# Optimization experiments

Measured on AMD Instinct MI355X. Metric: run time of the kernel, lower is better.

## Reference

```python
import jax, jax.numpy as jnp
import numpy as np

B, S, D_IN, D_OUT = 4, 2048, 1024, 1024


def setup_inputs() -> dict:
    key = jax.random.key(0)
    kx, kq, kk, kv = jax.random.split(key, 4)
    scale = 1.0 / np.sqrt(D_IN)
    return {
        "x": jax.random.normal(kx, (B, S, D_IN), dtype=jnp.float32),
        "W_q": jax.random.normal(kq, (D_IN, D_OUT), dtype=jnp.float32) * scale,
        "W_k": jax.random.normal(kk, (D_IN, D_OUT), dtype=jnp.float32) * scale,
        "W_v": jax.random.normal(kv, (D_IN, D_OUT), dtype=jnp.float32) * scale,
    }


def reference(x, W_q, W_k, W_v):
    # QKV projections (Linear without bias): [B,S,D_out]
    q = jnp.einsum("bsd,de->bse", x, W_q)
    k = jnp.einsum("bsd,de->bse", x, W_k)
    v = jnp.einsum("bsd,de->bse", x, W_v)

    # Raw scores [B,S,S], causal mask (strict upper triangle -> -inf),
    # then scale by sqrt(d_k) and softmax, matching the torch order of ops.
    scores = jnp.einsum("bqd,bkd->bqk", q, k)
    seq = scores.shape[-1]
    causal = jnp.triu(jnp.ones((seq, seq), dtype=bool), k=1)
    scores = jnp.where(causal[None, :, :], -jnp.inf, scores)
    attn = jax.nn.softmax(scores / jnp.sqrt(jnp.asarray(q.shape[-1], scores.dtype)), axis=-1)
    # dropout p=0.0 -> identity (eval semantics)
    return jnp.einsum("bqk,bkd->bqd", attn, v)
```

## Files before the change

### kernel.cpp

```cpp
#include <hip/hip_runtime.h>

typedef unsigned short u16;
typedef __bf16 bf16x8 __attribute__((ext_vector_type(8)));
typedef float f32x4 __attribute__((ext_vector_type(4)));

__device__ __forceinline__ u16 f2bf(float f) {
    union { float f; unsigned int u; } v; v.f = f;
    unsigned int u = v.u;
    return (u16)((u + 0x7FFFu + ((u >> 16) & 1u)) >> 16);
}

__device__ __forceinline__ void load_lds16(const void* g, void* l) {
    __builtin_amdgcn_global_load_lds(
        (const __attribute__((address_space(1))) unsigned int*)g,
        (__attribute__((address_space(3))) unsigned int*)l,
        16, 0, 0);
}

__global__ void __launch_bounds__(256) prep_kernel(
    const float4* __restrict__ X, u16* __restrict__ xb,
    const float* __restrict__ Wq, const float* __restrict__ Wk,
    const float* __restrict__ Wv,
    u16* __restrict__ Oq, u16* __restrict__ Ok, u16* __restrict__ Ov,
    float* __restrict__ rowsum) {
    __shared__ float tile[32][33];
    const int bid = blockIdx.x, tid = threadIdx.x;
    if (bid < 8192) {
        int idx = bid * 256 + tid;
        float4 v = X[idx];
        ushort4 o;
        o.x = f2bf(v.x); o.y = f2bf(v.y); o.z = f2bf(v.z); o.w = f2bf(v.w);
        *(ushort4*)(xb + (size_t)idx * 4) = o;
    } else if (bid < 11264) {
        int id = bid - 8192;
        int zz = id >> 10;
        const float* W = (zz == 0) ? Wq : (zz == 1) ? Wk : Wv;
        u16* O = (zz == 0) ? Oq : (zz == 1) ? Ok : Ov;
        int n0 = (id & 31) * 32, k0 = ((id >> 5) & 31) * 32;
        int tx = tid & 31, ty = tid >> 5;
        #pragma unroll
        for (int j = 0; j < 32; j += 8)
            tile[ty + j][tx] = W[(size_t)(k0 + ty + j) * 1024 + n0 + tx];
        __syncthreads();
        #pragma unroll
        for (int j = 0; j < 32; j += 8)
            O[(size_t)(n0 + ty + j) * 1024 + k0 + tx] = f2bf(tile[tx][ty + j]);
    } else {
        rowsum[(bid - 11264) * 256 + tid] = 0.f;
    }
}

__global__ void __launch_bounds__(512) gemm_qkv(
    const u16* __restrict__ xb, const u16* __restrict__ WqT,
    const u16* __restrict__ WkT, const u16* __restrict__ WvT,
    u16* __restrict__ Q, u16* __restrict__ Kb, u16* __restrict__ Vt) {

    int L = blockIdx.x;
    int c = L & 7, t = (L >> 3) & 7, hi = L >> 6;
    int p = hi * 8 + c;
    const int z = p >> 6, mtile = p & 63, ntile = t;
    const u16* A = xb;
    const u16* B = (z == 0) ? WqT : (z == 1) ? WkT : WvT;

    __shared__ __align__(16) u16 As[2 * 128 * 32];
    __shared__ __align__(16) u16 Bs[2 * 128 * 32];

    const int tid = threadIdx.x;
    const int lane = tid & 63;
    const int wave = tid >> 6;
    const int wr = wave >> 2, wc = wave & 3;

    const int r0 = tid >> 2;
    const int kb = (((tid & 3) ^ ((r0 >> 1) & 3))) * 16;

    const char* gA = (const char*)(A + (size_t)(mtile * 128 + r0) * 1024) + kb;
    const char* gB = (const char*)(B + (size_t)(ntile * 128 + r0) * 1024) + kb;
    char* lA = (char*)As + tid * 16;
    char* lB = (char*)Bs + tid * 16;

    f32x4 acc[4][2] = {};

    const int quad = lane >> 4;
    const int l16 = lane & 15;
    const int ch = quad ^ ((l16 >> 1) & 3);
    const int aoff = (wr * 64 + l16) * 32 + ch * 8;
    const int boff = (wc * 32 + l16) * 32 + ch * 8;

    for (int kt = 0; kt < 16; ++kt) {
        load_lds16(gA,      lA);
        load_lds16(gA + 64, lA + 8192);
        load_lds16(gB,      lB);
        load_lds16(gB + 64, lB + 8192);
        gA += 128; gB += 128;
        __syncthreads();
        #pragma unroll
        for (int h = 0; h < 2; ++h) {
            const u16* ap = As + h * 4096 + aoff;
            const u16* bp = Bs + h * 4096 + boff;
            bf16x8 af[4], bfv[2];
            #pragma unroll
            for (int r = 0; r < 4; ++r) af[r] = *(const bf16x8*)(ap + r * 512);
            #pragma unroll
            for (int cc = 0; cc < 2; ++cc) bfv[cc] = *(const bf16x8*)(bp + cc * 512);
            #pragma unroll
            for (int r = 0; r < 4; ++r)
                #pragma unroll
                for (int cc = 0; cc < 2; ++cc)
                    acc[r][cc] = __builtin_amdgcn_mfma_f32_16x16x32_bf16(
                        af[r], bfv[cc], acc[r][cc], 0, 0, 0);
        }
        __syncthreads();
    }

    const int grow0 = mtile * 128 + wr * 64 + quad * 4;
    const int gcol0 = ntile * 128 + wc * 32 + l16;

    if (z < 2) {
        u16* C = z ? Kb : Q;
        #pragma unroll
        for (int r = 0; r < 4; ++r)
            #pragma unroll
            for (int cc = 0; cc < 2; ++cc)
                #pragma unroll
                for (int i = 0; i < 4; ++i)
                    C[(size_t)(grow0 + r * 16 + i) * 1024 + gcol0 + cc * 16] =
                        f2bf(acc[r][cc][i]);
    } else {
        #pragma unroll
        for (int r = 0; r < 4; ++r) {
            int m0 = grow0 + r * 16;
            int b = m0 >> 11, s0 = m0 & 2047;
            #pragma unroll
            for (int cc = 0; cc < 2; ++cc) {
                int d = gcol0 + cc * 16;
                ushort4 o;
                o.x = f2bf(acc[r][cc][0]); o.y = f2bf(acc[r][cc][1]);
                o.z = f2bf(acc[r][cc][2]); o.w = f2bf(acc[r][cc][3]);
                *(ushort4*)(Vt + (size_t)b * (1024 * 2048) + (size_t)d * 2048 + s0) = o;
            }
        }
    }
}

template <int MODE>
__global__ void __launch_bounds__(256) gemm_small(
    const u16* __restrict__ Q, const u16* __restrict__ Kb,
    const u16* __restrict__ Vt, u16* __restrict__ S,
    float* __restrict__ rowsum, float* __restrict__ out) {

    int g, ntile, z, kiters;
    const u16 *A, *B;

    if (MODE == 1) {
        int L = blockIdx.x;
        int p = L & 63;
        g = L >> 6;
        z = p >> 4;
        ntile = p & 15;
        if (ntile > (g >> 1)) return;
        kiters = 16;
        A = Q  + (size_t)z * (2048 * 1024);
        B = Kb + (size_t)z * (2048 * 1024);
    } else {
        int L = blockIdx.x;
        int p = L & 31;
        g = 31 - (L >> 5);
        z = p >> 3;
        ntile = p & 7;
        kiters = g + 1;
        A = S  + (size_t)z * (2048 * 2048);
        B = Vt + (size_t)z * (1024 * 2048);
    }

    const int LD = (MODE == 2) ? 2048 : 1024;

    __shared__ __align__(16) u16 As[2 * 64 * 32];
    __shared__ __align__(16) u16 Bs[2 * 128 * 32];

    const int tid = threadIdx.x;
    const int lane = tid & 63;
    const int wc = tid >> 6;
    const int r0 = tid >> 2;
    const int kb = (((tid & 3) ^ ((r0 >> 1) & 3))) * 16;

    const char* gA  = (const char*)(A + (size_t)(g * 64 + r0) * LD) + kb;
    const char* gB0 = (const char*)(B + (size_t)(ntile * 128 + r0) * LD) + kb;
    const char* gB1 = gB0 + (size_t)64 * LD * 2;

    char* lA = (char*)As + tid * 16;
    char* lB = (char*)Bs + tid * 16;

    f32x4 acc[4][2] = {};

    const int quad = lane >> 4;
    const int l16 = lane & 15;
    const int ch = quad ^ ((l16 >> 1) & 3);
    const int aoff = l16 * 32 + ch * 8;
    const int boff = (wc * 32 + l16) * 32 + ch * 8;

    for (int kt = 0; kt < kiters; ++kt) {
        #pragma unroll
        for (int h = 0; h < 2; ++h) {
            load_lds16(gA  + h * 64, lA + h * 4096);
            load_lds16(gB0 + h * 64, lB + h * 8192);
            load_lds16(gB1 + h * 64, lB + h * 8192 + 4096);
        }
        gA += 128; gB0 += 128; gB1 += 128;
        __syncthreads();
        #pragma unroll
        for (int h = 0; h < 2; ++h) {
            const u16* ap = As + h * 2048 + aoff;
            const u16* bp = Bs + h * 4096 + boff;
            bf16x8 af[4], bfv[2];
            #pragma unroll
            for (int r = 0; r < 4; ++r) af[r] = *(const bf16x8*)(ap + r * 512);
            #pragma unroll
            for (int cc = 0; cc < 2; ++cc) bfv[cc] = *(const bf16x8*)(bp + cc * 512);
            #pragma unroll
            for (int r = 0; r < 4; ++r)
                #pragma unroll
                for (int cc = 0; cc < 2; ++cc)
                    acc[r][cc] = __builtin_amdgcn_mfma_f32_16x16x32_bf16(
                        af[r], bfv[cc], acc[r][cc], 0, 0, 0);
        }
        __syncthreads();
    }

    const int grow0 = g * 64 + quad * 4;
    const int gcol0 = ntile * 128 + wc * 32 + l16;

    if (MODE == 1) {
        u16* C = S + (size_t)z * (2048 * 2048);
        float* rs = rowsum + z * 2048;
        float rsum[4][4];
        #pragma unroll
        for (int r = 0; r < 4; ++r)
            #pragma unroll
            for (int i = 0; i < 4; ++i) rsum[r][i] = 0.f;
        #pragma unroll
        for (int r = 0; r < 4; ++r)
            #pragma unroll
            for (int cc = 0; cc < 2; ++cc)
                #pragma unroll
                for (int i = 0; i < 4; ++i) {
                    int grow = grow0 + r * 16 + i;
                    int gcol = gcol0 + cc * 16;
                    float e = (gcol <= grow)
                                  ? __expf(acc[r][cc][i] * 0.03125f - 12.0f)
                                  : 0.f;
                    C[(size_t)grow * 2048 + gcol] = f2bf(e);
                    rsum[r][i] += e;
                }
        #pragma unroll
        for (int r = 0; r < 4; ++r)
            #pragma unroll
            for (int i = 0; i < 4; ++i) {
                float s = rsum[r][i];
                s += __shfl_xor(s, 1, 64);
                s += __shfl_xor(s, 2, 64);
                s += __shfl_xor(s, 4, 64);
                s += __shfl_xor(s, 8, 64);
                if (l16 == 0)
                    atomicAdd(&rs[grow0 + r * 16 + i], s);
            }
    } else {
        const float* rs = rowsum + z * 2048;
        float* C = out + (size_t)z * (2048 * 1024);
        #pragma unroll
        for (int r = 0; r < 4; ++r)
            #pragma unroll
            for (int i = 0; i < 4; ++i) {
                int grow = grow0 + r * 16 + i;
                float inv = 1.0f / rs[grow];
                #pragma unroll
                for (int cc = 0; cc < 2; ++cc)
                    C[(size_t)grow * 1024 + gcol0 + cc * 16] = acc[r][cc][i] * inv;
            }
    }
}

extern "C" void kernel_launch(void* const* d_in, const int* in_sizes, int n_in,
                              void* d_out, int out_size, void* d_ws, size_t ws_size,
                              hipStream_t stream) {
    const float* x  = (const float*)d_in[0];
    const float* Wq = (const float*)d_in[1];
    const float* Wk = (const float*)d_in[2];
    const float* Wv = (const float*)d_in[3];
    float* out = (float*)d_out;
    char* ws = (char*)d_ws;
    const size_t Mi = 1u << 20;

    u16* xb  = (u16*)(ws);
    u16* WqT = (u16*)(ws + 16 * Mi);
    u16* WkT = (u16*)(ws + 18 * Mi);
    u16* WvT = (u16*)(ws + 20 * Mi);
    u16* Q   = (u16*)(ws + 22 * Mi);
    u16* Kb  = (u16*)(ws + 38 * Mi);
    u16* Vt  = (u16*)(ws + 54 * Mi);
    u16* S   = (u16*)(ws + 70 * Mi);
    float* rowsum = (float*)(ws + 102 * Mi);

    prep_kernel<<<11296, 256, 0, stream>>>(
        (const float4*)x, xb, Wq, Wk, Wv, WqT, WkT, WvT, rowsum);

    gemm_qkv<<<1536, 512, 0, stream>>>(xb, WqT, WkT, WvT, Q, Kb, Vt);

    gemm_small<1><<<2048, 256, 0, stream>>>(Q, Kb, Vt, S, rowsum, out);

    gemm_small<2><<<1024, 256, 0, stream>>>(Q, Kb, Vt, S, rowsum, out);
}
```

Before: 246.5 us.

## Split scores and PV into dedicated kernels with 128x128 tiles and balanced causal scheduling

Replaces the templated 64x128-tile gemm_small with two 512-thread kernels using 128x128 tiles. The scores kernel enumerates only the lower-triangular tiles (544 blocks) through a paired mapping, and applies the causal mask only on diagonal tiles. The PV kernel gives each block two complementary row tiles (mtile and 15-mtile) so every block does the same amount of causal work. The goals are fewer wasted blocks, better operand reuse per load and balanced load, at the cost of fewer blocks in flight and more LDS per block.

After: 225.1 us. -8.7%, faster.

```diff
diff --git a/kernel.cpp b/kernel.cpp
--- a/kernel.cpp
+++ b/kernel.cpp
@@ -142,51 +142,34 @@
     }
 }
 
-template <int MODE>
-__global__ void __launch_bounds__(256) gemm_small(
+__global__ void __launch_bounds__(512) gemm_scores(
     const u16* __restrict__ Q, const u16* __restrict__ Kb,
-    const u16* __restrict__ Vt, u16* __restrict__ S,
-    float* __restrict__ rowsum, float* __restrict__ out) {
-
-    int g, ntile, z, kiters;
-    const u16 *A, *B;
-
-    if (MODE == 1) {
-        int L = blockIdx.x;
-        int p = L & 63;
-        g = L >> 6;
-        z = p >> 4;
-        ntile = p & 15;
-        if (ntile > (g >> 1)) return;
-        kiters = 16;
-        A = Q  + (size_t)z * (2048 * 1024);
-        B = Kb + (size_t)z * (2048 * 1024);
-    } else {
-        int L = blockIdx.x;
-        int p = L & 31;
-        g = 31 - (L >> 5);
-        z = p >> 3;
-        ntile = p & 7;
-        kiters = g + 1;
-        A = S  + (size_t)z * (2048 * 2048);
-        B = Vt + (size_t)z * (1024 * 2048);
-    }
-
-    const int LD = (MODE == 2) ? 2048 : 1024;
-
-    __shared__ __align__(16) u16 As[2 * 64 * 32];
+    u16* __restrict__ S, float* __restrict__ rowsum) {
+
+    const int L = blockIdx.x;
+    const int c = L & 7;
+    const int q = L >> 3;
+    const int z = q / 17;
+    const int j = q - z * 17;
+    const int mtile = (j <= c) ? c : 15 - c;
+    const int ntile = (j <= c) ? j : j - c - 1;
+
+    const u16* A = Q  + (size_t)z * (2048 * 1024);
+    const u16* B = Kb + (size_t)z * (2048 * 1024);
+
+    __shared__ __align__(16) u16 As[2 * 128 * 32];
     __shared__ __align__(16) u16 Bs[2 * 128 * 32];
 
     const int tid = threadIdx.x;
     const int lane = tid & 63;
-    const int wc = tid >> 6;
+    const int wave = tid >> 6;
+    const int wr = wave >> 2, wc = wave & 3;
+
     const int r0 = tid >> 2;
     const int kb = (((tid & 3) ^ ((r0 >> 1) & 3))) * 16;
 
-    const char* gA  = (const char*)(A + (size_t)(g * 64 + r0) * LD) + kb;
-    const char* gB0 = (const char*)(B + (size_t)(ntile * 128 + r0) * LD) + kb;
-    const char* gB1 = gB0 + (size_t)64 * LD * 2;
-
+    const char* gA = (const char*)(A + (size_t)(mtile * 128 + r0) * 1024) + kb;
+    const char* gB = (const char*)(B + (size_t)(ntile * 128 + r0) * 1024) + kb;
     char* lA = (char*)As + tid * 16;
     char* lB = (char*)Bs + tid * 16;
 
@@ -195,21 +178,19 @@
     const int quad = lane >> 4;
     const int l16 = lane & 15;
     const int ch = quad ^ ((l16 >> 1) & 3);
-    const int aoff = l16 * 32 + ch * 8;
+    const int aoff = (wr * 64 + l16) * 32 + ch * 8;
     const int boff = (wc * 32 + l16) * 32 + ch * 8;
 
-    for (int kt = 0; kt < kiters; ++kt) {
+    for (int kt = 0; kt < 16; ++kt) {
+        load_lds16(gA,      lA);
+        load_lds16(gA + 64, lA + 8192);
+        load_lds16(gB,      lB);
+        load_lds16(gB + 64, lB + 8192);
+        gA += 128; gB += 128;
+        __syncthreads();
         #pragma unroll
         for (int h = 0; h < 2; ++h) {
-            load_lds16(gA  + h * 64, lA + h * 4096);
-            load_lds16(gB0 + h * 64, lB + h * 8192);
-            load_lds16(gB1 + h * 64, lB + h * 8192 + 4096);
-        }
-        gA += 128; gB0 += 128; gB1 += 128;
-        __syncthreads();
-        #pragma unroll
-        for (int h = 0; h < 2; ++h) {
-            const u16* ap = As + h * 2048 + aoff;
+            const u16* ap = As + h * 4096 + aoff;
             const u16* bp = Bs + h * 4096 + boff;
             bf16x8 af[4], bfv[2];
             #pragma unroll
@@ -226,46 +207,118 @@
         __syncthreads();
     }
 
-    const int grow0 = g * 64 + quad * 4;
+    const int grow0 = mtile * 128 + wr * 64 + quad * 4;
     const int gcol0 = ntile * 128 + wc * 32 + l16;
 
-    if (MODE == 1) {
-        u16* C = S + (size_t)z * (2048 * 2048);
-        float* rs = rowsum + z * 2048;
-        float rsum[4][4];
-        #pragma unroll
-        for (int r = 0; r < 4; ++r)
-            #pragma unroll
-            for (int i = 0; i < 4; ++i) rsum[r][i] = 0.f;
-        #pragma unroll
-        for (int r = 0; r < 4; ++r)
-            #pragma unroll
-            for (int cc = 0; cc < 2; ++cc)
-                #pragma unroll
-                for (int i = 0; i < 4; ++i) {
-                    int grow = grow0 + r * 16 + i;
-                    int gcol = gcol0 + cc * 16;
-                    float e = (gcol <= grow)
-                                  ? __expf(acc[r][cc][i] * 0.03125f - 12.0f)
-                                  : 0.f;
-                    C[(size_t)grow * 2048 + gcol] = f2bf(e);
-                    rsum[r][i] += e;
-                }
-        #pragma unroll
-        for (int r = 0; r < 4; ++r)
+    u16* C = S + (size_t)z * (2048 * 2048);
+    float* rs = rowsum + z * 2048;
+    const bool diag = (ntile == mtile);
+    float rsum[4][4];
+    #pragma unroll
+    for (int r = 0; r < 4; ++r)
+        #pragma unroll
+        for (int i = 0; i < 4; ++i) rsum[r][i] = 0.f;
+    #pragma unroll
+    for (int r = 0; r < 4; ++r)
+        #pragma unroll
+        for (int cc = 0; cc < 2; ++cc)
             #pragma unroll
             for (int i = 0; i < 4; ++i) {
-                float s = rsum[r][i];
-                s += __shfl_xor(s, 1, 64);
-                s += __shfl_xor(s, 2, 64);
-                s += __shfl_xor(s, 4, 64);
-                s += __shfl_xor(s, 8, 64);
-                if (l16 == 0)
-                    atomicAdd(&rs[grow0 + r * 16 + i], s);
+                int grow = grow0 + r * 16 + i;
+                int gcol = gcol0 + cc * 16;
+                float e = 0.f;
+                if (!diag || gcol <= grow)
+                    e = __expf(acc[r][cc][i] * 0.03125f - 12.0f);
+                C[(size_t)grow * 2048 + gcol] = f2bf(e);
+                rsum[r][i] += e;
             }
-    } else {
-        const float* rs = rowsum + z * 2048;
-        float* C = out + (size_t)z * (2048 * 1024);
+    #pragma unroll
+    for (int r = 0; r < 4; ++r)
+        #pragma unroll
+        for (int i = 0; i < 4; ++i) {
+            float s = rsum[r][i];
+            s += __shfl_xor(s, 1, 64);
+            s += __shfl_xor(s, 2, 64);
+            s += __shfl_xor(s, 4, 64);
+            s += __shfl_xor(s, 8, 64);
+            if (l16 == 0)
+                atomicAdd(&rs[grow0 + r * 16 + i], s);
+        }
+}
+
+__global__ void __launch_bounds__(512) gemm_pv(
+    const u16* __restrict__ S, const u16* __restrict__ Vt,
+    const float* __restrict__ rowsum, float* __restrict__ out) {
+
+    const int L = blockIdx.x;
+    const int ntile = L & 7;
+    const int x = L >> 3;
+    const int z = x & 3;
+    const int mp = x >> 2;
+
+    const u16* Abase = S  + (size_t)z * (2048 * 2048);
+    const u16* B     = Vt + (size_t)z * (1024 * 2048);
+    const float* rs  = rowsum + z * 2048;
+    float* C = out + (size_t)z * (2048 * 1024);
+
+    __shared__ __align__(16) u16 As[2 * 128 * 32];
+    __shared__ __align__(16) u16 Bs[2 * 128 * 32];
+
+    const int tid = threadIdx.x;
+    const int lane = tid & 63;
+    const int wave = tid >> 6;
+    const int wr = wave >> 2, wc = wave & 3;
+
+    const int r0 = tid >> 2;
+    const int kb = (((tid & 3) ^ ((r0 >> 1) & 3))) * 16;
+
+    char* lA = (char*)As + tid * 16;
+    char* lB = (char*)Bs + tid * 16;
+
+    const int quad = lane >> 4;
+    const int l16 = lane & 15;
+    const int ch = quad ^ ((l16 >> 1) & 3);
+    const int aoff = (wr * 64 + l16) * 32 + ch * 8;
+    const int boff = (wc * 32 + l16) * 32 + ch * 8;
+
+    #pragma unroll
+    for (int ti = 0; ti < 2; ++ti) {
+        const int mtile = ti ? mp : 15 - mp;
+        const int kiters = (mtile + 1) * 2;
+
+        const char* gA = (const char*)(Abase + (size_t)(mtile * 128 + r0) * 2048) + kb;
+        const char* gB = (const char*)(B + (size_t)(ntile * 128 + r0) * 2048) + kb;
+
+        f32x4 acc[4][2] = {};
+
+        for (int kt = 0; kt < kiters; ++kt) {
+            load_lds16(gA,      lA);
+            load_lds16(gA + 64, lA + 8192);
+            load_lds16(gB,      lB);
+            load_lds16(gB + 64, lB + 8192);
+            gA += 128; gB += 128;
+            __syncthreads();
+            #pragma unroll
+            for (int h = 0; h < 2; ++h) {
+                const u16* ap = As + h * 4096 + aoff;
+                const u16* bp = Bs + h * 4096 + boff;
+                bf16x8 af[4], bfv[2];
+                #pragma unroll
+                for (int r = 0; r < 4; ++r) af[r] = *(const bf16x8*)(ap + r * 512);
+                #pragma unroll
+                for (int cc = 0; cc < 2; ++cc) bfv[cc] = *(const bf16x8*)(bp + cc * 512);
+                #pragma unroll
+                for (int r = 0; r < 4; ++r)
+                    #pragma unroll
+                    for (int cc = 0; cc < 2; ++cc)
+                        acc[r][cc] = __builtin_amdgcn_mfma_f32_16x16x32_bf16(
+                            af[r], bfv[cc], acc[r][cc], 0, 0, 0);
+            }
+            __syncthreads();
+        }
+
+        const int grow0 = mtile * 128 + wr * 64 + quad * 4;
+        const int gcol0 = ntile * 128 + wc * 32 + l16;
         #pragma unroll
         for (int r = 0; r < 4; ++r)
             #pragma unroll
@@ -305,7 +358,7 @@
 
     gemm_qkv<<<1536, 512, 0, stream>>>(xb, WqT, WkT, WvT, Q, Kb, Vt);
 
-    gemm_small<1><<<2048, 256, 0, stream>>>(Q, Kb, Vt, S, rowsum, out);
-
-    gemm_small<2><<<1024, 256, 0, stream>>>(Q, Kb, Vt, S, rowsum, out);
-}
+    gemm_scores<<<544, 512, 0, stream>>>(Q, Kb, S, rowsum);
+
+    gemm_pv<<<256, 512, 0, stream>>>(S, Vt, rowsum, out);
+}
```
